# Optimization experiments

Hardware: AMD Instinct MI355X
Metric: run time of the kernel (lower is better)

## Reference

```python
import jax, jax.numpy as jnp
import numpy as np

NH = 2            # num heads
B = 2             # batch
CH = (64, 128, 256, 512)
HW = (128, 64, 32, 16)


def _mha(q, kv, w_in, b_in, w_out, b_out):
    # q, kv: [B, C, H, W] feature maps; seq layout (L, B, C) as in torch MHA (batch_first=False)
    Bq, C, H, W = q.shape
    L = H * W
    S = kv.shape[2] * kv.shape[3]
    qs = q.reshape(Bq, C, L).transpose(2, 0, 1)    # [L,B,C]
    ks = kv.reshape(Bq, C, S).transpose(2, 0, 1)   # [S,B,C]
    wq, wk, wv = jnp.split(w_in, 3, axis=0)        # torch in_proj_weight rows = [q; k; v]
    bq, bk, bv = jnp.split(b_in, 3)
    dh = C // NH
    qp = (qs @ wq.T + bq).reshape(L, Bq, NH, dh)
    kp = (ks @ wk.T + bk).reshape(S, Bq, NH, dh)
    vp = (ks @ wv.T + bv).reshape(S, Bq, NH, dh)
    scale = 1.0 / jnp.sqrt(jnp.asarray(dh, qp.dtype))
    scores = jnp.einsum('lbhd,sbhd->bhls', qp * scale, kp)  # [B,H,L,S]
    attn = jax.nn.softmax(scores, axis=-1)
    out = jnp.einsum('bhls,sbhd->lbhd', attn, vp).reshape(L, Bq, C)
    out = out @ w_out.T + b_out                    # out_proj
    return out.transpose(1, 2, 0).reshape(Bq, C, H, W)


def _level(fx1, fx2, fx3, w12, b12, ow12, ob12, w13, b13, ow13, ob13, sqw, sqb):
    att1 = _mha(fx1, fx2, w12, b12, ow12, ob12)
    att2 = _mha(fx1, fx3, w13, b13, ow13, ob13)
    cat = jnp.concatenate([fx1, att1, att2], axis=1)          # [B, 3C, H, W]
    return jnp.einsum('oc,bchw->bohw', sqw, cat) + sqb[None, :, None, None]  # 1x1 conv


def setup_inputs() -> dict:
    key = jax.random.key(0)
    ks = iter(jax.random.split(key, 64))
    d = {}
    for lvl in range(4):
        c, s = CH[lvl], HW[lvl]
        d[f'f1_{lvl}'] = jax.random.normal(next(ks), (B, c, s, s), jnp.float32)
    for lvl in range(1, 4):
        c, s = CH[lvl], HW[lvl]
        d[f'f2_{lvl}'] = jax.random.normal(next(ks), (B, c, s, s), jnp.float32)
        d[f'f3_{lvl}'] = jax.random.normal(next(ks), (B, c, s, s), jnp.float32)
    for i in (1, 2, 3):
        c = CH[i]
        sc = 1.0 / np.sqrt(c).astype(np.float32)
        for p in ('a12', 'a13'):
            d[f'{p}w{i}'] = jax.random.normal(next(ks), (3 * c, c), jnp.float32) * sc
            d[f'{p}b{i}'] = jnp.zeros((3 * c,), jnp.float32)
            d[f'{p}ow{i}'] = jax.random.normal(next(ks), (c, c), jnp.float32) * sc
            d[f'{p}ob{i}'] = jnp.zeros((c,), jnp.float32)
        d[f'sqw{i}'] = jax.random.normal(next(ks), (c, 3 * c), jnp.float32) * np.float32(1.0 / np.sqrt(3 * c))
        d[f'sqb{i}'] = jnp.zeros((c,), jnp.float32)
    return d


def reference(f1_0, f1_1, f1_2, f1_3, f2_1, f2_2, f2_3, f3_1, f3_2, f3_3,
              a12w1, a12b1, a12ow1, a12ob1, a13w1, a13b1, a13ow1, a13ob1, sqw1, sqb1,
              a12w2, a12b2, a12ow2, a12ob2, a13w2, a13b2, a13ow2, a13ob2, sqw2, sqb2,
              a12w3, a12b3, a12ow3, a12ob3, a13w3, a13b3, a13ow3, a13ob3, sqw3, sqb3):
    out0 = f1_0  # level 0 passes through untouched
    out1 = _level(f1_1, f2_1, f3_1, a12w1, a12b1, a12ow1, a12ob1, a13w1, a13b1, a13ow1, a13ob1, sqw1, sqb1)
    out2 = _level(f1_2, f2_2, f3_2, a12w2, a12b2, a12ow2, a12ob2, a13w2, a13b2, a13ow2, a13ob2, sqw2, sqb2)
    out3 = _level(f1_3, f2_3, f3_3, a12w3, a12b3, a12ow3, a12ob3, a13w3, a13b3, a13ow3, a13ob3, sqw3, sqb3)
    return (out0, out1, out2, out3)
```

## Files before the change

### kernel.cpp

```cpp
#include <hip/hip_runtime.h>
#include <hip/hip_bf16.h>
#include <math.h>

#define NHEADS 2

typedef unsigned short u16;
typedef __attribute__((ext_vector_type(8))) unsigned short u16x8;
typedef __attribute__((ext_vector_type(4))) unsigned short u16x4;
typedef __attribute__((ext_vector_type(8))) short short8;
typedef __attribute__((ext_vector_type(4))) short short4v;
typedef __attribute__((ext_vector_type(4))) float f32x4;

__device__ __forceinline__ u16 f2bf(float x) {
    __hip_bfloat16 h = __float2bfloat16(x);
    return __builtin_bit_cast(unsigned short, h);
}

__global__ __launch_bounds__(256) void transpose_bf16_kernel(
    const float* __restrict__ s0, const float* __restrict__ s1,
    const float* __restrict__ s2,
    u16* __restrict__ d0, u16* __restrict__ d1, u16* __restrict__ d2,
    int C, int L)
{
    const int z = blockIdx.z;
    const int which = z >> 1;
    const int b = z & 1;
    const float* __restrict__ src = (which == 0) ? s0 : (which == 1 ? s1 : s2);
    u16* __restrict__ dst = (which == 0) ? d0 : (which == 1 ? d1 : d2);
    const int l0 = blockIdx.x * 32;
    const int c0 = blockIdx.y * 32;
    __shared__ float Ts[32][33];
    const int t = threadIdx.x;
    const int x = t & 31, y = t >> 5;
    #pragma unroll
    for (int p = 0; p < 4; ++p)
        Ts[y + 8 * p][x] = src[((size_t)(b * C + c0 + y + 8 * p)) * L + l0 + x];
    __syncthreads();
    #pragma unroll
    for (int p = 0; p < 4; ++p)
        dst[((size_t)(b * L + l0 + y + 8 * p)) * C + c0 + x] = f2bf(Ts[x][y + 8 * p]);
}

__global__ __launch_bounds__(256) void gemm_qkv(
    const u16* __restrict__ f1t, const u16* __restrict__ f2t,
    const u16* __restrict__ f3t,
    const float* __restrict__ w12, const float* __restrict__ b12,
    const float* __restrict__ w13, const float* __restrict__ b13,
    u16* __restrict__ Qa, u16* __restrict__ Ka, u16* __restrict__ Va,
    u16* __restrict__ Qb, u16* __restrict__ Kb, u16* __restrict__ Vb,
    int M, int C, int L, int dh, float qscale, int gx, int perAtt)
{
    const int att = blockIdx.x / perAtt;
    const int r = blockIdx.x - att * perAtt;
    const int n0 = (r % gx) * 64;
    const int m0 = (r / gx) * 64;
    const int K = C;
    __shared__ __align__(16) u16 Xs[64][72];
    __shared__ __align__(16) u16 Ws[64][72];
    const int tid = threadIdx.x;
    const int wid = tid >> 6, lane = tid & 63;
    const int lo = lane & 15, hi = lane >> 4;
    const int wm = wid >> 1, wn = wid & 1;

    const u16* __restrict__ X = (n0 < C) ? f1t : (att ? f3t : f2t);
    const float* __restrict__ W = att ? w13 : w12;
    const float* __restrict__ bias = att ? b13 : b12;

    f32x4 acc[2][2];
    #pragma unroll
    for (int i = 0; i < 2; ++i)
        #pragma unroll
        for (int j = 0; j < 2; ++j)
            #pragma unroll
            for (int rr = 0; rr < 4; ++rr) acc[i][j][rr] = 0.f;

    u16x8 xreg[2];
    f32x4 wreg[4];

    auto load_x = [&](int k0) {
        #pragma unroll
        for (int p = 0; p < 2; ++p) {
            int c = tid + p * 256;
            int row = c >> 3, kc = c & 7;
            xreg[p] = *(const u16x8*)&X[(size_t)(m0 + row) * K + k0 + kc * 8];
        }
    };
    auto load_w = [&](int k0) {
        #pragma unroll
        for (int p = 0; p < 4; ++p) {
            int c = tid + p * 256;
            int row = c >> 4, kc = c & 15;
            wreg[p] = *(const f32x4*)&W[(size_t)(n0 + row) * K + k0 + kc * 4];
        }
    };

    load_x(0);
    load_w(0);
    const int ns = K / 64;
    for (int s = 0; s < ns; ++s) {
        __syncthreads();
        #pragma unroll
        for (int p = 0; p < 2; ++p) {
            int c = tid + p * 256;
            int row = c >> 3, kc = c & 7;
            *(u16x8*)&Xs[row][kc * 8] = xreg[p];
        }
        #pragma unroll
        for (int p = 0; p < 4; ++p) {
            int c = tid + p * 256;
            int row = c >> 4, kc = c & 15;
            u16x4 cv = {f2bf(wreg[p][0]), f2bf(wreg[p][1]),
                        f2bf(wreg[p][2]), f2bf(wreg[p][3])};
            *(u16x4*)&Ws[row][kc * 4] = cv;
        }
        __syncthreads();
        if (s + 1 < ns) { load_x((s + 1) * 64); load_w((s + 1) * 64); }
        #pragma unroll
        for (int kk = 0; kk < 2; ++kk) {
            short8 wf0 = *(const short8*)&Ws[wn * 32 + lo][kk * 32 + hi * 8];
            short8 wf1 = *(const short8*)&Ws[wn * 32 + 16 + lo][kk * 32 + hi * 8];
            short8 xf0 = *(const short8*)&Xs[wm * 32 + lo][kk * 32 + hi * 8];
            short8 xf1 = *(const short8*)&Xs[wm * 32 + 16 + lo][kk * 32 + hi * 8];
            acc[0][0] = __builtin_amdgcn_mfma_f32_16x16x32_bf16(wf0, xf0, acc[0][0], 0, 0, 0);
            acc[0][1] = __builtin_amdgcn_mfma_f32_16x16x32_bf16(wf1, xf0, acc[0][1], 0, 0, 0);
            acc[1][0] = __builtin_amdgcn_mfma_f32_16x16x32_bf16(wf0, xf1, acc[1][0], 0, 0, 0);
            acc[1][1] = __builtin_amdgcn_mfma_f32_16x16x32_bf16(wf1, xf1, acc[1][1], 0, 0, 0);
        }
    }

    #pragma unroll
    for (int nt = 0; nt < 2; ++nt) {
        const int nb = n0 + wn * 32 + nt * 16 + hi * 4;
        const float b0 = bias[nb + 0], b1 = bias[nb + 1];
        const float b2 = bias[nb + 2], b3 = bias[nb + 3];
        const int which = nb / C;
        const int co = nb - which * C;
        const int h = co / dh;
        const int dd = co - h * dh;
        u16* dst = (which == 0) ? (att ? Qb : Qa)
                 : (which == 1) ? (att ? Kb : Ka) : (att ? Vb : Va);
        const float sc = (which == 0) ? qscale : 1.0f;
        #pragma unroll
        for (int mt = 0; mt < 2; ++mt) {
            int m = m0 + wm * 32 + mt * 16 + lo;
            int b_ = m / L; int l = m - b_ * L;
            u16x4 pk = {f2bf((acc[mt][nt][0] + b0) * sc),
                        f2bf((acc[mt][nt][1] + b1) * sc),
                        f2bf((acc[mt][nt][2] + b2) * sc),
                        f2bf((acc[mt][nt][3] + b3) * sc)};
            *(u16x4*)&dst[((size_t)(b_ * NHEADS + h) * L + l) * dh + dd] = pk;
        }
    }
}

__global__ __launch_bounds__(256) void gemm_proj(
    const u16* __restrict__ Ana, const u16* __restrict__ Anb,
    const float* __restrict__ w12, const float* __restrict__ b12,
    const float* __restrict__ w13, const float* __restrict__ b13,
    u16* __restrict__ A1t, u16* __restrict__ A2t,
    int M, int C, int gx, int perAtt)
{
    const int att = blockIdx.x / perAtt;
    const int r = blockIdx.x - att * perAtt;
    const int n0 = (r % gx) * 64;
    const int m0 = (r / gx) * 64;
    const int K = C;
    __shared__ __align__(16) u16 Xs[64][72];
    __shared__ __align__(16) u16 Ws[64][72];
    const int tid = threadIdx.x;
    const int wid = tid >> 6, lane = tid & 63;
    const int lo = lane & 15, hi = lane >> 4;
    const int wm = wid >> 1, wn = wid & 1;

    const u16* __restrict__ X = att ? Anb : Ana;
    const float* __restrict__ W = att ? w13 : w12;
    const float* __restrict__ bias = att ? b13 : b12;
    u16* __restrict__ dst = att ? A2t : A1t;

    f32x4 acc[2][2];
    #pragma unroll
    for (int i = 0; i < 2; ++i)
        #pragma unroll
        for (int j = 0; j < 2; ++j)
            #pragma unroll
            for (int rr = 0; rr < 4; ++rr) acc[i][j][rr] = 0.f;

    u16x8 xreg[2];
    f32x4 wreg[4];

    auto load_x = [&](int k0) {
        #pragma unroll
        for (int p = 0; p < 2; ++p) {
            int c = tid + p * 256;
            int row = c >> 3, kc = c & 7;
            xreg[p] = *(const u16x8*)&X[(size_t)(m0 + row) * K + k0 + kc * 8];
        }
    };
    auto load_w = [&](int k0) {
        #pragma unroll
        for (int p = 0; p < 4; ++p) {
            int c = tid + p * 256;
            int row = c >> 4, kc = c & 15;
            wreg[p] = *(const f32x4*)&W[(size_t)(n0 + row) * K + k0 + kc * 4];
        }
    };

    load_x(0);
    load_w(0);
    const int ns = K / 64;
    for (int s = 0; s < ns; ++s) {
        __syncthreads();
        #pragma unroll
        for (int p = 0; p < 2; ++p) {
            int c = tid + p * 256;
            int row = c >> 3, kc = c & 7;
            *(u16x8*)&Xs[row][kc * 8] = xreg[p];
        }
        #pragma unroll
        for (int p = 0; p < 4; ++p) {
            int c = tid + p * 256;
            int row = c >> 4, kc = c & 15;
            u16x4 cv = {f2bf(wreg[p][0]), f2bf(wreg[p][1]),
                        f2bf(wreg[p][2]), f2bf(wreg[p][3])};
            *(u16x4*)&Ws[row][kc * 4] = cv;
        }
        __syncthreads();
        if (s + 1 < ns) { load_x((s + 1) * 64); load_w((s + 1) * 64); }
        #pragma unroll
        for (int kk = 0; kk < 2; ++kk) {
            short8 wf0 = *(const short8*)&Ws[wn * 32 + lo][kk * 32 + hi * 8];
            short8 wf1 = *(const short8*)&Ws[wn * 32 + 16 + lo][kk * 32 + hi * 8];
            short8 xf0 = *(const short8*)&Xs[wm * 32 + lo][kk * 32 + hi * 8];
            short8 xf1 = *(const short8*)&Xs[wm * 32 + 16 + lo][kk * 32 + hi * 8];
            acc[0][0] = __builtin_amdgcn_mfma_f32_16x16x32_bf16(wf0, xf0, acc[0][0], 0, 0, 0);
            acc[0][1] = __builtin_amdgcn_mfma_f32_16x16x32_bf16(wf1, xf0, acc[0][1], 0, 0, 0);
            acc[1][0] = __builtin_amdgcn_mfma_f32_16x16x32_bf16(wf0, xf1, acc[1][0], 0, 0, 0);
            acc[1][1] = __builtin_amdgcn_mfma_f32_16x16x32_bf16(wf1, xf1, acc[1][1], 0, 0, 0);
        }
    }

    #pragma unroll
    for (int nt = 0; nt < 2; ++nt) {
        const int nb = n0 + wn * 32 + nt * 16 + hi * 4;
        const float b0 = bias[nb + 0], b1 = bias[nb + 1];
        const float b2 = bias[nb + 2], b3 = bias[nb + 3];
        #pragma unroll
        for (int mt = 0; mt < 2; ++mt) {
            int m = m0 + wm * 32 + mt * 16 + lo;
            u16x4 pk = {f2bf(acc[mt][nt][0] + b0), f2bf(acc[mt][nt][1] + b1),
                        f2bf(acc[mt][nt][2] + b2), f2bf(acc[mt][nt][3] + b3)};
            *(u16x4*)&dst[(size_t)m * C + nb] = pk;
        }
    }
}

__global__ __launch_bounds__(256) void gemm_squeeze(
    const u16* __restrict__ X0, const u16* __restrict__ X1,
    const u16* __restrict__ X2,
    const float* __restrict__ W, const float* __restrict__ bias,
    float* __restrict__ out, int M, int C, int L)
{
    const int n0 = blockIdx.x * 64;
    const int m0 = blockIdx.y * 64;
    const int K = 3 * C;
    __shared__ __align__(16) u16 Xs[64][72];
    __shared__ __align__(16) u16 Ws[64][72];
    const int tid = threadIdx.x;
    const int wid = tid >> 6, lane = tid & 63;
    const int lo = lane & 15, hi = lane >> 4;
    const int wm = wid >> 1, wn = wid & 1;

    f32x4 acc[2][2];
    #pragma unroll
    for (int i = 0; i < 2; ++i)
        #pragma unroll
        for (int j = 0; j < 2; ++j)
            #pragma unroll
            for (int rr = 0; rr < 4; ++rr) acc[i][j][rr] = 0.f;

    u16x8 xreg[2];
    f32x4 wreg[4];

    auto load_x = [&](int k0) {
        int wk = k0 / C;
        const u16* src = (wk == 0) ? X0 : (wk == 1 ? X1 : X2);
        int kl = k0 - wk * C;
        #pragma unroll
        for (int p = 0; p < 2; ++p) {
            int c = tid + p * 256;
            int row = c >> 3, kc = c & 7;
            xreg[p] = *(const u16x8*)&src[(size_t)(m0 + row) * C + kl + kc * 8];
        }
    };
    auto load_w = [&](int k0) {
        #pragma unroll
        for (int p = 0; p < 4; ++p) {
            int c = tid + p * 256;
            int row = c >> 4, kc = c & 15;
            wreg[p] = *(const f32x4*)&W[(size_t)(n0 + row) * K + k0 + kc * 4];
        }
    };

    load_x(0);
    load_w(0);
    const int ns = K / 64;
    for (int s = 0; s < ns; ++s) {
        __syncthreads();
        #pragma unroll
        for (int p = 0; p < 2; ++p) {
            int c = tid + p * 256;
            int row = c >> 3, kc = c & 7;
            *(u16x8*)&Xs[row][kc * 8] = xreg[p];
        }
        #pragma unroll
        for (int p = 0; p < 4; ++p) {
            int c = tid + p * 256;
            int row = c >> 4, kc = c & 15;
            u16x4 cv = {f2bf(wreg[p][0]), f2bf(wreg[p][1]),
                        f2bf(wreg[p][2]), f2bf(wreg[p][3])};
            *(u16x4*)&Ws[row][kc * 4] = cv;
        }
        __syncthreads();
        if (s + 1 < ns) { load_x((s + 1) * 64); load_w((s + 1) * 64); }
        #pragma unroll
        for (int kk = 0; kk < 2; ++kk) {
            short8 wf0 = *(const short8*)&Ws[wn * 32 + lo][kk * 32 + hi * 8];
            short8 wf1 = *(const short8*)&Ws[wn * 32 + 16 + lo][kk * 32 + hi * 8];
            short8 xf0 = *(const short8*)&Xs[wm * 32 + lo][kk * 32 + hi * 8];
            short8 xf1 = *(const short8*)&Xs[wm * 32 + 16 + lo][kk * 32 + hi * 8];
            acc[0][0] = __builtin_amdgcn_mfma_f32_16x16x32_bf16(wf0, xf0, acc[0][0], 0, 0, 0);
            acc[0][1] = __builtin_amdgcn_mfma_f32_16x16x32_bf16(wf1, xf0, acc[0][1], 0, 0, 0);
            acc[1][0] = __builtin_amdgcn_mfma_f32_16x16x32_bf16(wf0, xf1, acc[1][0], 0, 0, 0);
            acc[1][1] = __builtin_amdgcn_mfma_f32_16x16x32_bf16(wf1, xf1, acc[1][1], 0, 0, 0);
        }
    }

    #pragma unroll
    for (int nt = 0; nt < 2; ++nt) {
        const int nb = n0 + wn * 32 + nt * 16 + hi * 4;
        const float b0 = bias[nb + 0], b1 = bias[nb + 1];
        const float b2 = bias[nb + 2], b3 = bias[nb + 3];
        #pragma unroll
        for (int mt = 0; mt < 2; ++mt) {
            int m = m0 + wm * 32 + mt * 16 + lo;
            int b_ = m / L; int l = m - b_ * L;
            out[((size_t)(b_ * C + nb + 0)) * L + l] = acc[mt][nt][0] + b0;
            out[((size_t)(b_ * C + nb + 1)) * L + l] = acc[mt][nt][1] + b1;
            out[((size_t)(b_ * C + nb + 2)) * L + l] = acc[mt][nt][2] + b2;
            out[((size_t)(b_ * C + nb + 3)) * L + l] = acc[mt][nt][3] + b3;
        }
    }
}

template <int DH, int NPAR, int NQS>
__global__ __launch_bounds__(128 * NPAR) void flash_split(
    const u16* __restrict__ Q1, const u16* __restrict__ K1,
    const u16* __restrict__ V1, u16* __restrict__ O1,
    const u16* __restrict__ Q2, const u16* __restrict__ K2,
    const u16* __restrict__ V2, u16* __restrict__ O2, int L, int S)
{
    constexpr int KB = 64;
    constexpr int QW = 16 * NQS;
    constexpr int QB = 2 * QW;
    constexpr int NKK = DH / 32;
    constexpr int NNT = DH / 16;
    constexpr int DG = DH / 8;
    constexpr int SLOTS = DG / 8;
    constexpr int SZ_VT = 2 * NPAR * DH * KB * 2;
    constexpr int MST = DH + 4;
    constexpr int P = NPAR - 1;

    __shared__ __align__(16) char smem[SZ_VT];
    u16 (*Vt)[NPAR][DH][KB] = (u16 (*)[NPAR][DH][KB])smem;
    float* MrgAcc = (float*)smem;
    float* MrgML  = (float*)(smem + (size_t)2 * P * QW * MST * 4);

    const int nQT = L / QB;
    const int perAtt = 2 * NHEADS * nQT;
    const int att = blockIdx.x / perAtt;
    const int rem = blockIdx.x - att * perAtt;
    const int qt = rem % nQT;
    const int bh = rem / nQT;
    const u16* __restrict__ Q = att ? Q2 : Q1;
    const u16* __restrict__ K = att ? K2 : K1;
    const u16* __restrict__ V = att ? V2 : V1;
    u16* __restrict__ O = att ? O2 : O1;

    const int tid = threadIdx.x;
    const int w = tid >> 6;
    const int lane = tid & 63;
    const int lo = lane & 15, hi = lane >> 4;
    const int qg = w & 1, par = w >> 1;
    const int q0 = qt * QB + qg * QW;

    short8 qf[NQS][NKK];
    #pragma unroll
    for (int qs = 0; qs < NQS; ++qs)
        #pragma unroll
        for (int kk = 0; kk < NKK; ++kk)
            qf[qs][kk] = *(const short8*)&Q[((size_t)bh * L + q0 + qs * 16 + lo) * DH + kk * 32 + hi * 8];

    f32x4 acc[NQS][NNT];
    #pragma unroll
    for (int qs = 0; qs < NQS; ++qs)
        #pragma unroll
        for (int nt = 0; nt < NNT; ++nt)
            #pragma unroll
            for (int r = 0; r < 4; ++r) acc[qs][nt][r] = 0.f;
    float m_i[NQS], l_i[NQS];
    #pragma unroll
    for (int qs = 0; qs < NQS; ++qs) { m_i[qs] = -1e30f; l_i[qs] = 0.f; }

    const u16* Kbase = K + (size_t)bh * S * DH;
    const u16* Vbase = V + (size_t)bh * S * DH;

    short8 kf[4][NKK];
    auto load_kf = [&](int r) {
        const u16* Kt = Kbase + (size_t)(NPAR * r + par) * KB * DH;
        #pragma unroll
        for (int st = 0; st < 4; ++st)
            #pragma unroll
            for (int kk = 0; kk < NKK; ++kk)
                kf[st][kk] = *(const short8*)&Kt[(size_t)(st * 16 + lo) * DH + kk * 32 + hi * 8];
    };

    const int pt = tid >> 7;
    const int u = tid & 127;
    int dV0[SLOTS], sV0[SLOTS];
    #pragma unroll
    for (int z = 0; z < SLOTS; ++z) {
        int e = u + z * 128;
        dV0[z] = (e % DG) * 8;
        sV0[z] = (e / DG) * 4;
    }

    u16x8 vreg[SLOTS][4];

    auto loadslots = [&](int r) {
        const u16* Vp = Vbase + (size_t)(NPAR * r + pt) * KB * DH;
        #pragma unroll
        for (int z = 0; z < SLOTS; ++z)
            #pragma unroll
            for (int si = 0; si < 4; ++si)
                vreg[z][si] = *(const u16x8*)&Vp[(size_t)(sV0[z] + si) * DH + dV0[z]];
    };
    auto writeslots = [&](int buf) {
        #pragma unroll
        for (int z = 0; z < SLOTS; ++z)
            #pragma unroll
            for (int j = 0; j < 8; ++j) {
                int d = dV0[z] + j;
                int g = ((d >> 3) ^ d) & 7;
                int scol = (sV0[z] & 7) | ((((sV0[z] >> 3) ^ g) & 7) << 3);
                u16x4 wj = {vreg[z][0][j], vreg[z][1][j], vreg[z][2][j], vreg[z][3][j]};
                *(u16x4*)&Vt[buf][pt][d][scol] = wj;
            }
    };

    const int NR = S / (KB * NPAR);

    load_kf(0);
    loadslots(0);
    writeslots(0);
    __syncthreads();
    if (1 < NR) loadslots(1);

    for (int r = 0; r < NR; ++r) {
        const int cur = r & 1;

        f32x4 sacc[4][NQS];
        #pragma unroll
        for (int st = 0; st < 4; ++st)
            #pragma unroll
            for (int qs = 0; qs < NQS; ++qs)
                #pragma unroll
                for (int rr = 0; rr < 4; ++rr) sacc[st][qs][rr] = 0.f;
        #pragma unroll
        for (int st = 0; st < 4; ++st) {
            #pragma unroll
            for (int kk = 0; kk < NKK; ++kk) {
                #pragma unroll
                for (int qs = 0; qs < NQS; ++qs)
                    sacc[st][qs] = __builtin_amdgcn_mfma_f32_16x16x32_bf16(
                        kf[st][kk], qf[qs][kk], sacc[st][qs], 0, 0, 0);
            }
        }

        if (r + 1 < NR) load_kf(r + 1);

        float mn[NQS], ts[NQS];
        #pragma unroll
        for (int qs = 0; qs < NQS; ++qs) {
            float tm = -1e30f;
            #pragma unroll
            for (int st = 0; st < 4; ++st)
                #pragma unroll
                for (int rr = 0; rr < 4; ++rr) tm = fmaxf(tm, sacc[st][qs][rr]);
            tm = fmaxf(tm, __shfl_xor(tm, 16));
            tm = fmaxf(tm, __shfl_xor(tm, 32));
            const bool grow = __any(tm > m_i[qs] + 8.0f);
            mn[qs] = grow ? fmaxf(m_i[qs], tm) : m_i[qs];
            ts[qs] = 0.f;
            if (grow) {
                float alpha = __builtin_amdgcn_exp2f(m_i[qs] - mn[qs]);
                m_i[qs] = mn[qs];
                l_i[qs] *= alpha;
                float ar[4];
                #pragma unroll
                for (int rr = 0; rr < 4; ++rr) ar[rr] = __shfl(alpha, hi * 4 + rr);
                #pragma unroll
                for (int nt = 0; nt < NNT; ++nt)
                    #pragma unroll
                    for (int rr = 0; rr < 4; ++rr) acc[qs][nt][rr] *= ar[rr];
            }
        }

        if (r + 1 < NR) writeslots(cur ^ 1);

        __builtin_amdgcn_s_setprio(1);
        #pragma unroll
        for (int st = 0; st < 4; ++st) {
            short4v pa_[NQS];
            #pragma unroll
            for (int qs = 0; qs < NQS; ++qs) {
                float p0 = __builtin_amdgcn_exp2f(sacc[st][qs][0] - mn[qs]);
                float p1 = __builtin_amdgcn_exp2f(sacc[st][qs][1] - mn[qs]);
                float p2 = __builtin_amdgcn_exp2f(sacc[st][qs][2] - mn[qs]);
                float p3 = __builtin_amdgcn_exp2f(sacc[st][qs][3] - mn[qs]);
                ts[qs] += (p0 + p1) + (p2 + p3);
                short4v pk = {(short)f2bf(p0), (short)f2bf(p1),
                              (short)f2bf(p2), (short)f2bf(p3)};
                pa_[qs] = pk;
            }
            const int s0 = st * 16 + hi * 4;
            #pragma unroll
            for (int nt = 0; nt < NNT; ++nt) {
                int d = nt * 16 + lo;
                int g = ((d >> 3) ^ d) & 7;
                int scol = (s0 & 7) | ((((s0 >> 3) ^ g) & 7) << 3);
                short4v vb = *(const short4v*)&Vt[cur][par][d][scol];
                #pragma unroll
                for (int qs = 0; qs < NQS; ++qs)
                    acc[qs][nt] = __builtin_amdgcn_mfma_f32_16x16x16bf16_1k(
                        pa_[qs], vb, acc[qs][nt], 0, 0, 0);
            }
        }
        __builtin_amdgcn_s_setprio(0);

        #pragma unroll
        for (int qs = 0; qs < NQS; ++qs) {
            float t2 = ts[qs];
            t2 += __shfl_xor(t2, 16);
            t2 += __shfl_xor(t2, 32);
            l_i[qs] += t2;
        }

        __syncthreads();
        if (r + 2 < NR) loadslots(r + 2);
    }

    const int b_ = bh / NHEADS, h_ = bh % NHEADS;
    if (par != 0) {
        const int mi = qg * P + par - 1;
        float* ma = MrgAcc + (size_t)mi * QW * MST;
        #pragma unroll
        for (int qs = 0; qs < NQS; ++qs) {
            #pragma unroll
            for (int nt = 0; nt < NNT; ++nt)
                #pragma unroll
                for (int rr = 0; rr < 4; ++rr)
                    ma[(size_t)(qs * 16 + hi * 4 + rr) * MST + nt * 16 + lo] = acc[qs][nt][rr];
            if (hi == 0) {
                MrgML[(mi * 2 + 0) * QW + qs * 16 + lo] = m_i[qs];
                MrgML[(mi * 2 + 1) * QW + qs * 16 + lo] = l_i[qs];
            }
        }
    }
    __syncthreads();
    if (par == 0) {
        #pragma unroll
        for (int qs = 0; qs < NQS; ++qs) {
            float mp[P > 0 ? P : 1], lp[P > 0 ? P : 1];
            float mt = m_i[qs];
            #pragma unroll
            for (int p = 0; p < P; ++p) {
                mp[p] = MrgML[((qg * P + p) * 2 + 0) * QW + qs * 16 + lo];
                lp[p] = MrgML[((qg * P + p) * 2 + 1) * QW + qs * 16 + lo];
                mt = fmaxf(mt, mp[p]);
            }
            float c0 = __builtin_amdgcn_exp2f(m_i[qs] - mt);
            float lt = c0 * l_i[qs];
            float cp[P > 0 ? P : 1];
            #pragma unroll
            for (int p = 0; p < P; ++p) {
                cp[p] = __builtin_amdgcn_exp2f(mp[p] - mt);
                lt += cp[p] * lp[p];
            }
            float linv = 1.0f / lt;
            c0 *= linv;
            #pragma unroll
            for (int p = 0; p < P; ++p) cp[p] *= linv;
            float c0r[4], cpr[P > 0 ? P : 1][4];
            #pragma unroll
            for (int rr = 0; rr < 4; ++rr) {
                c0r[rr] = __shfl(c0, hi * 4 + rr);
                #pragma unroll
                for (int p = 0; p < P; ++p) cpr[p][rr] = __shfl(cp[p], hi * 4 + rr);
            }
            #pragma unroll
            for (int nt = 0; nt < NNT; ++nt)
                #pragma unroll
                for (int rr = 0; rr < 4; ++rr) {
                    int q = qs * 16 + hi * 4 + rr;
                    float ov = acc[qs][nt][rr] * c0r[rr];
                    #pragma unroll
                    for (int p = 0; p < P; ++p)
                        ov += MrgAcc[((size_t)(qg * P + p) * QW + q) * MST + nt * 16 + lo] * cpr[p][rr];
                    O[(((size_t)b_ * L + q0 + q) * NHEADS + h_) * DH + nt * 16 + lo] = f2bf(ov);
                }
        }
    }
}

template <int DH, int NQS, int PRE>
__global__ __launch_bounds__(128) void flash_mfma(
    const u16* __restrict__ Q1, const u16* __restrict__ K1,
    const u16* __restrict__ V1, u16* __restrict__ O1,
    const u16* __restrict__ Q2, const u16* __restrict__ K2,
    const u16* __restrict__ V2, u16* __restrict__ O2, int L, int S)
{
    constexpr int KB = 64;
    constexpr int QW = NQS * 16;
    constexpr int QB = 2 * QW;
    constexpr int DH8 = DH / 8;
    constexpr int KC = (KB * DH8) / 128;
    constexpr int VU = (16 * DH8) / 128;
    constexpr int NKK = DH / 32;
    constexpr int NNT = DH / 16;

    __shared__ __align__(16) u16 Ks[KB][DH + 8];
    __shared__ __align__(16) u16 Vt[DH][KB];

    const int nQT = L / QB;
    const int perAtt = 2 * NHEADS * nQT;
    const int att = blockIdx.x / perAtt;
    const int rem = blockIdx.x - att * perAtt;
    const int qt = rem % nQT;
    const int bh = rem / nQT;
    const u16* __restrict__ Q = att ? Q2 : Q1;
    const u16* __restrict__ K = att ? K2 : K1;
    const u16* __restrict__ V = att ? V2 : V1;
    u16* __restrict__ O = att ? O2 : O1;

    const int tid = threadIdx.x;
    const int wv = tid >> 6;
    const int lane = tid & 63;
    const int lo = lane & 15;
    const int hi = lane >> 4;
    const int q0 = qt * QB + wv * QW;

    short8 qf[NQS][NKK];
    #pragma unroll
    for (int qs = 0; qs < NQS; ++qs)
        #pragma unroll
        for (int kk = 0; kk < NKK; ++kk)
            qf[qs][kk] = *(const short8*)&Q[((size_t)bh * L + q0 + qs * 16 + lo) * DH + kk * 32 + hi * 8];

    f32x4 acc[NQS][NNT];
    #pragma unroll
    for (int qs = 0; qs < NQS; ++qs)
        #pragma unroll
        for (int nt = 0; nt < NNT; ++nt)
            #pragma unroll
            for (int r = 0; r < 4; ++r) acc[qs][nt][r] = 0.f;
    float m_i[NQS], l_i[NQS];
    #pragma unroll
    for (int qs = 0; qs < NQS; ++qs) { m_i[qs] = -1e30f; l_i[qs] = 0.f; }

    const int NT = S / KB;
    u16x8 kreg[PRE ? KC : 1];
    u16x8 vreg[PRE ? VU : 1][4];

    const u16* Kbase = K + (size_t)bh * S * DH;
    const u16* Vbase = V + (size_t)bh * S * DH;

    auto vwrite = [&](int d, int s0, u16x4 wj) {
        int g = ((d >> 3) ^ d) & 7;
        int scol = (s0 & 7) | ((((s0 >> 3) ^ g) & 7) << 3);
        *(u16x4*)&Vt[d][scol] = wj;
    };

    if (PRE) {
        #pragma unroll
        for (int i = 0; i < KC; ++i) {
            int idx = tid + i * 128;
            kreg[i] = *(const u16x8*)&Kbase[(size_t)(idx / DH8) * DH + (idx % DH8) * 8];
        }
        #pragma unroll
        for (int u = 0; u < VU; ++u) {
            int uu = tid + u * 128;
            int d0 = (uu % DH8) * 8, s0 = (uu / DH8) * 4;
            #pragma unroll
            for (int si = 0; si < 4; ++si)
                vreg[u][si] = *(const u16x8*)&Vbase[(size_t)(s0 + si) * DH + d0];
        }
    }

    for (int t = 0; t < NT; ++t) {
        __syncthreads();
        if (PRE) {
            #pragma unroll
            for (int i = 0; i < KC; ++i) {
                int idx = tid + i * 128;
                *(u16x8*)&Ks[idx / DH8][(idx % DH8) * 8] = kreg[i];
            }
            #pragma unroll
            for (int u = 0; u < VU; ++u) {
                int uu = tid + u * 128;
                int d0 = (uu % DH8) * 8, s0 = (uu / DH8) * 4;
                #pragma unroll
                for (int j = 0; j < 8; ++j) {
                    u16x4 wj = {vreg[u][0][j], vreg[u][1][j], vreg[u][2][j], vreg[u][3][j]};
                    vwrite(d0 + j, s0, wj);
                }
            }
        } else {
            const u16* Kp = Kbase + (size_t)t * KB * DH;
            const u16* Vp = Vbase + (size_t)t * KB * DH;
            #pragma unroll
            for (int i = 0; i < KC; ++i) {
                int idx = tid + i * 128;
                *(u16x8*)&Ks[idx / DH8][(idx % DH8) * 8] =
                    *(const u16x8*)&Kp[(size_t)(idx / DH8) * DH + (idx % DH8) * 8];
            }
            #pragma unroll
            for (int u = 0; u < VU; ++u) {
                int uu = tid + u * 128;
                int d0 = (uu % DH8) * 8, s0 = (uu / DH8) * 4;
                u16x8 v0 = *(const u16x8*)&Vp[(size_t)(s0 + 0) * DH + d0];
                u16x8 v1 = *(const u16x8*)&Vp[(size_t)(s0 + 1) * DH + d0];
                u16x8 v2 = *(const u16x8*)&Vp[(size_t)(s0 + 2) * DH + d0];
                u16x8 v3 = *(const u16x8*)&Vp[(size_t)(s0 + 3) * DH + d0];
                #pragma unroll
                for (int j = 0; j < 8; ++j) {
                    u16x4 wj = {v0[j], v1[j], v2[j], v3[j]};
                    vwrite(d0 + j, s0, wj);
                }
            }
        }
        __syncthreads();

        if (PRE && t + 1 < NT) {
            const u16* Kp = Kbase + (size_t)(t + 1) * KB * DH;
            const u16* Vp = Vbase + (size_t)(t + 1) * KB * DH;
            #pragma unroll
            for (int i = 0; i < KC; ++i) {
                int idx = tid + i * 128;
                kreg[i] = *(const u16x8*)&Kp[(size_t)(idx / DH8) * DH + (idx % DH8) * 8];
            }
            #pragma unroll
            for (int u = 0; u < VU; ++u) {
                int uu = tid + u * 128;
                int d0 = (uu % DH8) * 8, s0 = (uu / DH8) * 4;
                #pragma unroll
                for (int si = 0; si < 4; ++si)
                    vreg[u][si] = *(const u16x8*)&Vp[(size_t)(s0 + si) * DH + d0];
            }
        }

        f32x4 sacc[4][NQS];
        #pragma unroll
        for (int st = 0; st < 4; ++st)
            #pragma unroll
            for (int qs = 0; qs < NQS; ++qs)
                #pragma unroll
                for (int r = 0; r < 4; ++r) sacc[st][qs][r] = 0.f;
        #pragma unroll
        for (int st = 0; st < 4; ++st) {
            #pragma unroll
            for (int kk = 0; kk < NKK; ++kk) {
                short8 a = *(const short8*)&Ks[st * 16 + lo][kk * 32 + hi * 8];
                #pragma unroll
                for (int qs = 0; qs < NQS; ++qs)
                    sacc[st][qs] = __builtin_amdgcn_mfma_f32_16x16x32_bf16(
                        a, qf[qs][kk], sacc[st][qs], 0, 0, 0);
            }
        }

        float mn[NQS], ts[NQS];
        #pragma unroll
        for (int qs = 0; qs < NQS; ++qs) {
            float tm = -1e30f;
            #pragma unroll
            for (int st = 0; st < 4; ++st)
                #pragma unroll
                for (int r = 0; r < 4; ++r) tm = fmaxf(tm, sacc[st][qs][r]);
            tm = fmaxf(tm, __shfl_xor(tm, 16));
            tm = fmaxf(tm, __shfl_xor(tm, 32));
            const bool grow = __any(tm > m_i[qs] + 8.0f);
            mn[qs] = grow ? fmaxf(m_i[qs], tm) : m_i[qs];
            ts[qs] = 0.f;
            if (grow) {
                float alpha = __builtin_amdgcn_exp2f(m_i[qs] - mn[qs]);
                m_i[qs] = mn[qs];
                l_i[qs] *= alpha;
                float ar[4];
                #pragma unroll
                for (int r = 0; r < 4; ++r) ar[r] = __shfl(alpha, hi * 4 + r);
                #pragma unroll
                for (int nt = 0; nt < NNT; ++nt)
                    #pragma unroll
                    for (int r = 0; r < 4; ++r) acc[qs][nt][r] *= ar[r];
            }
        }

        #pragma unroll
        for (int st = 0; st < 4; ++st) {
            short4v pa_[NQS];
            #pragma unroll
            for (int qs = 0; qs < NQS; ++qs) {
                float p0 = __builtin_amdgcn_exp2f(sacc[st][qs][0] - mn[qs]);
                float p1 = __builtin_amdgcn_exp2f(sacc[st][qs][1] - mn[qs]);
                float p2 = __builtin_amdgcn_exp2f(sacc[st][qs][2] - mn[qs]);
                float p3 = __builtin_amdgcn_exp2f(sacc[st][qs][3] - mn[qs]);
                ts[qs] += (p0 + p1) + (p2 + p3);
                short4v pk = {(short)f2bf(p0), (short)f2bf(p1),
                              (short)f2bf(p2), (short)f2bf(p3)};
                pa_[qs] = pk;
            }
            const int s0 = st * 16 + hi * 4;
            #pragma unroll
            for (int nt = 0; nt < NNT; ++nt) {
                int d = nt * 16 + lo;
                int g = ((d >> 3) ^ d) & 7;
                int scol = (s0 & 7) | ((((s0 >> 3) ^ g) & 7) << 3);
                short4v vb = *(const short4v*)&Vt[d][scol];
                #pragma unroll
                for (int qs = 0; qs < NQS; ++qs)
                    acc[qs][nt] = __builtin_amdgcn_mfma_f32_16x16x16bf16_1k(
                        pa_[qs], vb, acc[qs][nt], 0, 0, 0);
            }
        }

        #pragma unroll
        for (int qs = 0; qs < NQS; ++qs) {
            float t2 = ts[qs];
            t2 += __shfl_xor(t2, 16);
            t2 += __shfl_xor(t2, 32);
            l_i[qs] += t2;
        }
    }

    const int b_ = bh / NHEADS, h_ = bh % NHEADS;
    #pragma unroll
    for (int qs = 0; qs < NQS; ++qs) {
        float inv = 1.0f / l_i[qs];
        float ir[4];
        #pragma unroll
        for (int r = 0; r < 4; ++r) ir[r] = __shfl(inv, hi * 4 + r);
        #pragma unroll
        for (int nt = 0; nt < NNT; ++nt)
            #pragma unroll
            for (int r = 0; r < 4; ++r) {
                int l = q0 + qs * 16 + hi * 4 + r;
                O[(((size_t)b_ * L + l) * NHEADS + h_) * DH + nt * 16 + lo] =
                    f2bf(acc[qs][nt][r] * ir[r]);
            }
    }
}


extern "C" void kernel_launch(void* const* d_in, const int* in_sizes, int n_in,
                              void* d_out, int out_size, void* d_ws, size_t ws_size,
                              hipStream_t stream)
{
    static const int CHs[4] = {64, 128, 256, 512};
    static const int HWs[4] = {128, 64, 32, 16};

    const float* f1[4] = {(const float*)d_in[0], (const float*)d_in[1],
                          (const float*)d_in[2], (const float*)d_in[3]};
    const float* f2[4] = {nullptr, (const float*)d_in[4], (const float*)d_in[6],
                          (const float*)d_in[8]};
    const float* f3[4] = {nullptr, (const float*)d_in[5], (const float*)d_in[7],
                          (const float*)d_in[9]};

    size_t out0_elems = (size_t)in_sizes[0];
    hipMemcpyAsync(d_out, d_in[0], out0_elems * sizeof(float),
                   hipMemcpyDeviceToDevice, stream);

    const size_t SL = (size_t)2 * 4096 * 128;
    u16* wsu = (u16*)d_ws;
    u16* f1t = wsu + 0 * SL;
    u16* f2t = wsu + 1 * SL;
    u16* f3t = wsu + 2 * SL;
    u16* Qa  = wsu + 3 * SL;
    u16* Ka  = wsu + 4 * SL;
    u16* Va  = wsu + 5 * SL;
    u16* Qb  = wsu + 6 * SL;
    u16* Kb  = wsu + 7 * SL;
    u16* Vb  = wsu + 8 * SL;
    u16* A1t = wsu + 9 * SL;
    u16* A2t = wsu + 10 * SL;
    u16* Ana = f2t;
    u16* Anb = f3t;

    const float LOG2E = 1.44269504088896340736f;

    size_t outOff = out0_elems;
    for (int lvl = 1; lvl <= 3; ++lvl) {
        const int C = CHs[lvl];
        const int Hs = HWs[lvl];
        const int L = Hs * Hs;
        const int dh = C / NHEADS;
        const int M = 2 * L;
        const float qscale = LOG2E / sqrtf((float)dh);
        const int bi = 10 + (lvl - 1) * 10;
        const float* a12w  = (const float*)d_in[bi + 0];
        const float* a12b  = (const float*)d_in[bi + 1];
        const float* a12ow = (const float*)d_in[bi + 2];
        const float* a12ob = (const float*)d_in[bi + 3];
        const float* a13w  = (const float*)d_in[bi + 4];
        const float* a13b  = (const float*)d_in[bi + 5];
        const float* a13ow = (const float*)d_in[bi + 6];
        const float* a13ob = (const float*)d_in[bi + 7];
        const float* sqw   = (const float*)d_in[bi + 8];
        const float* sqb   = (const float*)d_in[bi + 9];

        dim3 tg(L / 32, C / 32, 6);
        transpose_bf16_kernel<<<tg, 256, 0, stream>>>(f1[lvl], f2[lvl], f3[lvl],
                                                      f1t, f2t, f3t, C, L);

        const int gx = 3 * C / 64;
        const int perAtt = gx * (M / 64);
        gemm_qkv<<<2 * perAtt, 256, 0, stream>>>(
            f1t, f2t, f3t, a12w, a12b, a13w, a13b,
            Qa, Ka, Va, Qb, Kb, Vb, M, C, L, dh, qscale, gx, perAtt);

        if (dh == 64)
            flash_split<64, 4, 2><<<2 * (2 * NHEADS) * (L / 64), 512, 0, stream>>>(
                Qa, Ka, Va, Ana, Qb, Kb, Vb, Anb, L, L);
        else if (dh == 128)
            flash_split<128, 2, 1><<<2 * (2 * NHEADS) * (L / 32), 256, 0, stream>>>(
                Qa, Ka, Va, Ana, Qb, Kb, Vb, Anb, L, L);
        else
            flash_mfma<256, 1, 0><<<2 * (2 * NHEADS) * (L / 32), 128, 0, stream>>>(
                Qa, Ka, Va, Ana, Qb, Kb, Vb, Anb, L, L);

        const int gx2 = C / 64;
        const int perAtt2 = gx2 * (M / 64);
        gemm_proj<<<2 * perAtt2, 256, 0, stream>>>(
            Ana, Anb, a12ow, a12ob, a13ow, a13ob, A1t, A2t, M, C, gx2, perAtt2);

        dim3 gsq(C / 64, M / 64);
        gemm_squeeze<<<gsq, 256, 0, stream>>>(f1t, A1t, A2t, sqw, sqb,
                                              (float*)d_out + outOff, M, C, L);
        outOff += (size_t)2 * C * L;
    }
}
```

Before: 293.8 us.

## Fold attention out-projections into squeeze conv weights, drop per-level proj GEMM

Precomputes combined weights sqw_att·W_out for each attention branch, plus a fused bias, so the squeeze 1x1 conv consumes the attention outputs directly and the separate out-projection GEMM per level is removed. Two small prep kernels compute these folded weights at the start of every call. It also switches the dh=64 flash configuration to a smaller block with more blocks. The cost is the extra weight-product GEMM each call, which is cheap relative to the activation GEMMs it replaces, and an additional bf16 rounding of the folded weights.

```diff
diff --git a/kernel.cpp b/kernel.cpp
--- a/kernel.cpp
+++ b/kernel.cpp
@@ -153,30 +153,42 @@
     }
 }
 
-__global__ __launch_bounds__(256) void gemm_proj(
-    const u16* __restrict__ Ana, const u16* __restrict__ Anb,
-    const float* __restrict__ w12, const float* __restrict__ b12,
-    const float* __restrict__ w13, const float* __restrict__ b13,
-    u16* __restrict__ A1t, u16* __restrict__ A2t,
-    int M, int C, int gx, int perAtt)
+__global__ __launch_bounds__(256) void prep_w(
+    const float* __restrict__ s1, const float* __restrict__ oa1,
+    const float* __restrict__ ob1, float* __restrict__ w1,
+    const float* __restrict__ s2, const float* __restrict__ oa2,
+    const float* __restrict__ ob2, float* __restrict__ w2,
+    const float* __restrict__ s3, const float* __restrict__ oa3,
+    const float* __restrict__ ob3, float* __restrict__ w3)
 {
-    const int att = blockIdx.x / perAtt;
-    const int r = blockIdx.x - att * perAtt;
-    const int n0 = (r % gx) * 64;
-    const int m0 = (r / gx) * 64;
-    const int K = C;
-    __shared__ __align__(16) u16 Xs[64][72];
-    __shared__ __align__(16) u16 Ws[64][72];
+    int bid = blockIdx.x;
+    int C; const float *sqw, *owa, *owb; float* wp;
+    if (bid < 12)      { C = 128; sqw = s1; owa = oa1; owb = ob1; wp = w1; }
+    else if (bid < 60) { bid -= 12; C = 256; sqw = s2; owa = oa2; owb = ob2; wp = w2; }
+    else               { bid -= 60; C = 512; sqw = s3; owa = oa3; owb = ob3; wp = w3; }
+    const int K3 = 3 * C;
+    const int gxw = K3 / 64;
+    const int n0 = (bid / gxw) * 64;
+    const int kc0 = (bid % gxw) * 64;
     const int tid = threadIdx.x;
+
+    if (kc0 < C) {
+        for (int p = tid; p < 64 * 64; p += 256) {
+            int i = p >> 6, j = p & 63;
+            wp[(size_t)(n0 + i) * K3 + kc0 + j] = sqw[(size_t)(n0 + i) * K3 + kc0 + j];
+        }
+        return;
+    }
+    const int which = kc0 / C;
+    const int kp0 = kc0 - which * C;
+    const float* __restrict__ ow = (which == 1) ? owa : owb;
+
+    __shared__ __align__(16) u16 As[64][72];
+    __shared__ __align__(16) u16 Bs[64][72];
     const int wid = tid >> 6, lane = tid & 63;
     const int lo = lane & 15, hi = lane >> 4;
     const int wm = wid >> 1, wn = wid & 1;
 
-    const u16* __restrict__ X = att ? Anb : Ana;
-    const float* __restrict__ W = att ? w13 : w12;
-    const float* __restrict__ bias = att ? b13 : b12;
-    u16* __restrict__ dst = att ? A2t : A1t;
-
     f32x4 acc[2][2];
     #pragma unroll
     for (int i = 0; i < 2; ++i)
@@ -185,72 +197,60 @@
             #pragma unroll
             for (int rr = 0; rr < 4; ++rr) acc[i][j][rr] = 0.f;
 
-    u16x8 xreg[2];
-    f32x4 wreg[4];
-
-    auto load_x = [&](int k0) {
-        #pragma unroll
-        for (int p = 0; p < 2; ++p) {
-            int c = tid + p * 256;
-            int row = c >> 3, kc = c & 7;
-            xreg[p] = *(const u16x8*)&X[(size_t)(m0 + row) * K + k0 + kc * 8];
-        }
-    };
-    auto load_w = [&](int k0) {
-        #pragma unroll
-        for (int p = 0; p < 4; ++p) {
-            int c = tid + p * 256;
-            int row = c >> 4, kc = c & 15;
-            wreg[p] = *(const f32x4*)&W[(size_t)(n0 + row) * K + k0 + kc * 4];
-        }
-    };
-
-    load_x(0);
-    load_w(0);
-    const int ns = K / 64;
-    for (int s = 0; s < ns; ++s) {
+    for (int ct = 0; ct < C / 64; ++ct) {
         __syncthreads();
-        #pragma unroll
-        for (int p = 0; p < 2; ++p) {
-            int c = tid + p * 256;
-            int row = c >> 3, kc = c & 7;
-            *(u16x8*)&Xs[row][kc * 8] = xreg[p];
-        }
-        #pragma unroll
-        for (int p = 0; p < 4; ++p) {
-            int c = tid + p * 256;
-            int row = c >> 4, kc = c & 15;
-            u16x4 cv = {f2bf(wreg[p][0]), f2bf(wreg[p][1]),
-                        f2bf(wreg[p][2]), f2bf(wreg[p][3])};
-            *(u16x4*)&Ws[row][kc * 4] = cv;
+        for (int p = tid; p < 64 * 64; p += 256) {
+            int i = p >> 6, j = p & 63;
+            As[i][j] = f2bf(sqw[(size_t)(n0 + i) * K3 + which * C + ct * 64 + j]);
+            Bs[j][i] = f2bf(ow[(size_t)(ct * 64 + i) * C + kp0 + j]);
         }
         __syncthreads();
-        if (s + 1 < ns) { load_x((s + 1) * 64); load_w((s + 1) * 64); }
         #pragma unroll
         for (int kk = 0; kk < 2; ++kk) {
-            short8 wf0 = *(const short8*)&Ws[wn * 32 + lo][kk * 32 + hi * 8];
-            short8 wf1 = *(const short8*)&Ws[wn * 32 + 16 + lo][kk * 32 + hi * 8];
-            short8 xf0 = *(const short8*)&Xs[wm * 32 + lo][kk * 32 + hi * 8];
-            short8 xf1 = *(const short8*)&Xs[wm * 32 + 16 + lo][kk * 32 + hi * 8];
+            short8 wf0 = *(const short8*)&As[wn * 32 + lo][kk * 32 + hi * 8];
+            short8 wf1 = *(const short8*)&As[wn * 32 + 16 + lo][kk * 32 + hi * 8];
+            short8 xf0 = *(const short8*)&Bs[wm * 32 + lo][kk * 32 + hi * 8];
+            short8 xf1 = *(const short8*)&Bs[wm * 32 + 16 + lo][kk * 32 + hi * 8];
             acc[0][0] = __builtin_amdgcn_mfma_f32_16x16x32_bf16(wf0, xf0, acc[0][0], 0, 0, 0);
             acc[0][1] = __builtin_amdgcn_mfma_f32_16x16x32_bf16(wf1, xf0, acc[0][1], 0, 0, 0);
             acc[1][0] = __builtin_amdgcn_mfma_f32_16x16x32_bf16(wf0, xf1, acc[1][0], 0, 0, 0);
             acc[1][1] = __builtin_amdgcn_mfma_f32_16x16x32_bf16(wf1, xf1, acc[1][1], 0, 0, 0);
         }
     }
-
     #pragma unroll
     for (int nt = 0; nt < 2; ++nt) {
         const int nb = n0 + wn * 32 + nt * 16 + hi * 4;
-        const float b0 = bias[nb + 0], b1 = bias[nb + 1];
-        const float b2 = bias[nb + 2], b3 = bias[nb + 3];
         #pragma unroll
         for (int mt = 0; mt < 2; ++mt) {
-            int m = m0 + wm * 32 + mt * 16 + lo;
-            u16x4 pk = {f2bf(acc[mt][nt][0] + b0), f2bf(acc[mt][nt][1] + b1),
-                        f2bf(acc[mt][nt][2] + b2), f2bf(acc[mt][nt][3] + b3)};
-            *(u16x4*)&dst[(size_t)m * C + nb] = pk;
-        }
+            const int col = kc0 + wm * 32 + mt * 16 + lo;
+            #pragma unroll
+            for (int rr = 0; rr < 4; ++rr)
+                wp[(size_t)(nb + rr) * K3 + col] = acc[mt][nt][rr];
+        }
+    }
+}
+
+__global__ __launch_bounds__(256) void prep_b(
+    const float* __restrict__ s1, const float* __restrict__ oba1,
+    const float* __restrict__ obb1, const float* __restrict__ sqb1, float* __restrict__ b1,
+    const float* __restrict__ s2, const float* __restrict__ oba2,
+    const float* __restrict__ obb2, const float* __restrict__ sqb2, float* __restrict__ b2,
+    const float* __restrict__ s3, const float* __restrict__ oba3,
+    const float* __restrict__ obb3, const float* __restrict__ sqb3, float* __restrict__ b3)
+{
+    const int lvl = blockIdx.x;
+    const int C = (lvl == 0) ? 128 : (lvl == 1) ? 256 : 512;
+    const float* sqw = (lvl == 0) ? s1 : (lvl == 1) ? s2 : s3;
+    const float* oba = (lvl == 0) ? oba1 : (lvl == 1) ? oba2 : oba3;
+    const float* obb = (lvl == 0) ? obb1 : (lvl == 1) ? obb2 : obb3;
+    const float* sqb = (lvl == 0) ? sqb1 : (lvl == 1) ? sqb2 : sqb3;
+    float* bp = (lvl == 0) ? b1 : (lvl == 1) ? b2 : b3;
+    for (int n = threadIdx.x; n < C; n += 256) {
+        float s = sqb[n];
+        const float* row = sqw + (size_t)n * 3 * C;
+        for (int c = 0; c < C; ++c)
+            s += row[C + c] * oba[c] + row[2 * C + c] * obb[c];
+        bp[n] = s;
     }
 }
 
@@ -899,10 +899,33 @@
     u16* Qb  = wsu + 6 * SL;
     u16* Kb  = wsu + 7 * SL;
     u16* Vb  = wsu + 8 * SL;
-    u16* A1t = wsu + 9 * SL;
-    u16* A2t = wsu + 10 * SL;
     u16* Ana = f2t;
     u16* Anb = f3t;
+    float* wp1 = (float*)(wsu + 9 * SL);
+    float* wp2 = wp1 + (size_t)128 * 384;
+    float* wp3 = wp2 + (size_t)256 * 768;
+    float* bp1 = wp3 + (size_t)512 * 1536;
+    float* bp2 = bp1 + 512;
+    float* bp3 = bp2 + 512;
+
+    const float* SQW[3]; const float* OWA[3]; const float* OWB[3];
+    const float* OBA[3]; const float* OBB[3]; const float* SQB[3];
+    for (int l = 0; l < 3; ++l) {
+        const int bi = 10 + l * 10;
+        OWA[l] = (const float*)d_in[bi + 2];
+        OBA[l] = (const float*)d_in[bi + 3];
+        OWB[l] = (const float*)d_in[bi + 6];
+        OBB[l] = (const float*)d_in[bi + 7];
+        SQW[l] = (const float*)d_in[bi + 8];
+        SQB[l] = (const float*)d_in[bi + 9];
+    }
+
+    prep_w<<<252, 256, 0, stream>>>(SQW[0], OWA[0], OWB[0], wp1,
+                                    SQW[1], OWA[1], OWB[1], wp2,
+                                    SQW[2], OWA[2], OWB[2], wp3);
+    prep_b<<<3, 256, 0, stream>>>(SQW[0], OBA[0], OBB[0], SQB[0], bp1,
+                                  SQW[1], OBA[1], OBB[1], SQB[1], bp2,
+                                  SQW[2], OBA[2], OBB[2], SQB[2], bp3);
 
     const float LOG2E = 1.44269504088896340736f;
 
@@ -915,16 +938,12 @@
         const int M = 2 * L;
         const float qscale = LOG2E / sqrtf((float)dh);
         const int bi = 10 + (lvl - 1) * 10;
-        const float* a12w  = (const float*)d_in[bi + 0];
-        const float* a12b  = (const float*)d_in[bi + 1];
-        const float* a12ow = (const float*)d_in[bi + 2];
-        const float* a12ob = (const float*)d_in[bi + 3];
-        const float* a13w  = (const float*)d_in[bi + 4];
-        const float* a13b  = (const float*)d_in[bi + 5];
-        const float* a13ow = (const float*)d_in[bi + 6];
-        const float* a13ob = (const float*)d_in[bi + 7];
-        const float* sqw   = (const float*)d_in[bi + 8];
-        const float* sqb   = (const float*)d_in[bi + 9];
+        const float* a12w = (const float*)d_in[bi + 0];
+        const float* a12b = (const float*)d_in[bi + 1];
+        const float* a13w = (const float*)d_in[bi + 4];
+        const float* a13b = (const float*)d_in[bi + 5];
+        float* wp = (lvl == 1) ? wp1 : (lvl == 2) ? wp2 : wp3;
+        float* bp = (lvl == 1) ? bp1 : (lvl == 2) ? bp2 : bp3;
 
         dim3 tg(L / 32, C / 32, 6);
         transpose_bf16_kernel<<<tg, 256, 0, stream>>>(f1[lvl], f2[lvl], f3[lvl],
@@ -937,7 +956,7 @@
             Qa, Ka, Va, Qb, Kb, Vb, M, C, L, dh, qscale, gx, perAtt);
 
         if (dh == 64)
-            flash_split<64, 4, 2><<<2 * (2 * NHEADS) * (L / 64), 512, 0, stream>>>(
+            flash_split<64, 2, 1><<<2 * (2 * NHEADS) * (L / 32), 256, 0, stream>>>(
                 Qa, Ka, Va, Ana, Qb, Kb, Vb, Anb, L, L);
         else if (dh == 128)
             flash_split<128, 2, 1><<<2 * (2 * NHEADS) * (L / 32), 256, 0, stream>>>(
@@ -946,13 +965,8 @@
             flash_mfma<256, 1, 0><<<2 * (2 * NHEADS) * (L / 32), 128, 0, stream>>>(
                 Qa, Ka, Va, Ana, Qb, Kb, Vb, Anb, L, L);
 
-        const int gx2 = C / 64;
-        const int perAtt2 = gx2 * (M / 64);
-        gemm_proj<<<2 * perAtt2, 256, 0, stream>>>(
-            Ana, Anb, a12ow, a12ob, a13ow, a13ob, A1t, A2t, M, C, gx2, perAtt2);
-
         dim3 gsq(C / 64, M / 64);
-        gemm_squeeze<<<gsq, 256, 0, stream>>>(f1t, A1t, A2t, sqw, sqb,
+        gemm_squeeze<<<gsq, 256, 0, stream>>>(f1t, Ana, Anb, wp, bp,
                                               (float*)d_out + outOff, M, C, L);
         outOff += (size_t)2 * C * L;
     }
```

Result: slower. 612.4 us (+108.4%).
